# Performance work log

Measured on AMD Instinct MI355X. Metric: run time of the kernel, lower is better.

Reference implementation:

```python
import jax, jax.numpy as jnp
import numpy as np

D_MODEL = 1024
N_HEADS = 16
D_HEAD = D_MODEL // N_HEADS


def setup_inputs() -> dict:
    key = jax.random.key(0)
    ks = jax.random.split(key, 7)
    x = jax.random.normal(ks[0], (1, 4096, D_MODEL), dtype=jnp.float32)
    # torch Linear default init ~ U(-1/sqrt(fan_in), 1/sqrt(fan_in)); small randn is fine for a reference
    Wqkv = jax.random.normal(ks[1], (3 * D_MODEL, D_MODEL), dtype=jnp.float32) * (1.0 / np.sqrt(D_MODEL))
    bqkv = jax.random.normal(ks[2], (3 * D_MODEL,), dtype=jnp.float32) * 0.01
    Wo = jax.random.normal(ks[3], (D_MODEL, D_MODEL), dtype=jnp.float32) * (1.0 / np.sqrt(D_MODEL))
    bo = jax.random.normal(ks[4], (D_MODEL,), dtype=jnp.float32) * 0.01
    wq = jnp.ones((D_HEAD,), dtype=jnp.float32)
    wk = jnp.ones((D_HEAD,), dtype=jnp.float32)
    return {"x": x, "Wqkv": Wqkv, "bqkv": bqkv, "Wo": Wo, "bo": bo, "wq": wq, "wk": wk}


def _rmsnorm(x, w):
    # matches RMSNormRef: mean of squares over last dim, eps added to mean before sqrt
    xf = x.astype(jnp.float32)
    rms = jnp.mean(xf * xf, axis=-1, keepdims=True)
    return (xf / jnp.sqrt(rms + 1e-6) * w.astype(jnp.float32)).astype(x.dtype)


def reference(x, Wqkv, bqkv, Wo, bo, wq, wk):
    b, s, d = x.shape
    qkv = x @ Wqkv.T + bqkv                       # [b, s, 3d]
    q, k, v = jnp.split(qkv, 3, axis=-1)
    q = q.reshape(b, s, N_HEADS, D_HEAD)
    k = k.reshape(b, s, N_HEADS, D_HEAD)
    v = v.reshape(b, s, N_HEADS, D_HEAD)
    q = _rmsnorm(q, wq)
    k = _rmsnorm(k, wk)
    # NOTE: original applies NO 1/sqrt(d_head) scaling and NO causal mask
    qf = q.astype(jnp.float32)
    kf = k.astype(jnp.float32)
    vf = v.astype(jnp.float32)
    attn = jnp.einsum('bqhd,bkhd->bhqk', qf, kf)  # [b, h, s, s] fp32 scores
    attn = jax.nn.softmax(attn, axis=-1)
    z = jnp.einsum('bhqk,bkhd->bqhd', attn, vf).astype(x.dtype)
    z = z.reshape(b, s, d)
    return z @ Wo.T + bo
```

## Files before the change

### kernel.cpp

```cpp
#include <hip/hip_runtime.h>
#include <hip/hip_bf16.h>

typedef __bf16 bf16;
typedef bf16 bf16x8 __attribute__((ext_vector_type(8)));
typedef bf16 bf16x4 __attribute__((ext_vector_type(4)));
typedef float f32x4 __attribute__((ext_vector_type(4)));
typedef float f32x16 __attribute__((ext_vector_type(16)));
typedef unsigned int u32;
typedef u32 u32x4 __attribute__((ext_vector_type(4)));

static constexpr int SEQ    = 4096;
static constexpr int DMODEL = 1024;
static constexpr int NHEADS = 16;
static constexpr int DHEAD  = 64;
static constexpr int QKV3   = 3 * DMODEL;
static constexpr float SMAX = 64.0f;
static constexpr float LOG2E = 1.44269504088896341f;

__device__ inline void gld16(const bf16* g, bf16* l) {
    __builtin_amdgcn_global_load_lds(
        (const __attribute__((address_space(1))) void*)g,
        (__attribute__((address_space(3))) void*)l, 16, 0, 0);
}

__device__ inline bf16x8 load8(const float* src) {
    float4 a = *(const float4*)(src);
    float4 b = *(const float4*)(src + 4);
    bf16x8 r;
    r[0] = (bf16)a.x; r[1] = (bf16)a.y; r[2] = (bf16)a.z; r[3] = (bf16)a.w;
    r[4] = (bf16)b.x; r[5] = (bf16)b.y; r[6] = (bf16)b.z; r[7] = (bf16)b.w;
    return r;
}

__device__ inline f32x16 zero16() {
    f32x16 r;
#pragma unroll
    for (int i = 0; i < 16; ++i) r[i] = 0.f;
    return r;
}

static constexpr size_t NX = (size_t)SEQ * DMODEL;
static constexpr size_t NW = (size_t)QKV3 * DMODEL;
static constexpr size_t NO = (size_t)DMODEL * DMODEL;

__global__ __launch_bounds__(256)
void cvt_all(const float* __restrict__ x, const float* __restrict__ Wqkv,
             const float* __restrict__ Wo, bf16* __restrict__ outbase) {
    const size_t e = ((size_t)blockIdx.x * 256 + threadIdx.x) * 8;
    const float* src;
    if (e < NX)            src = x + e;
    else if (e < NX + NW)  src = Wqkv + (e - NX);
    else                   src = Wo + (e - NX - NW);
    *(bf16x8*)(outbase + e) = load8(src);
}

__global__ __launch_bounds__(256)
void gemm_qkv(const bf16* __restrict__ A, const bf16* __restrict__ W,
              const float* __restrict__ bias, const float* __restrict__ wq,
              const float* __restrict__ wk, bf16* __restrict__ qkv,
              bf16* __restrict__ Vt) {
    __shared__ __align__(16) bf16 As[128 * 32];
    __shared__ __align__(16) bf16 Ws[128 * 32];
    const int tid  = threadIdx.x;
    const int wave = tid >> 6;
    const int ll   = tid & 15;
    const int quad = (tid & 63) >> 4;
    const int wm   = (wave >> 1) * 64;
    const int wn   = (wave & 1) * 64;
    const int m0 = blockIdx.y * 128;
    const int n0 = blockIdx.x * 128;

    f32x4 acc[4][4];
#pragma unroll
    for (int i = 0; i < 4; ++i)
#pragma unroll
        for (int j = 0; j < 4; ++j) acc[i][j] = (f32x4){0.f, 0.f, 0.f, 0.f};

    for (int k0 = 0; k0 < DMODEL; k0 += 32) {
        __syncthreads();
#pragma unroll
        for (int i = 0; i < 2; ++i) {
            const int idx = i * 256 + tid;
            const int row = idx >> 2;
            const int c   = (idx & 3) ^ ((row >> 1) & 3);
            gld16(&A[(size_t)(m0 + row) * DMODEL + k0 + c * 8], As + idx * 8);
            gld16(&W[(size_t)(n0 + row) * DMODEL + k0 + c * 8], Ws + idx * 8);
        }
        __syncthreads();
        bf16x8 af[4], bfr[4];
#pragma unroll
        for (int mi = 0; mi < 4; ++mi) {
            const int row = wm + mi * 16 + ll;
            af[mi] = *(const bf16x8*)(As + (row * 4 + (quad ^ ((ll >> 1) & 3))) * 8);
        }
#pragma unroll
        for (int ni = 0; ni < 4; ++ni) {
            const int row = wn + ni * 16 + ll;
            bfr[ni] = *(const bf16x8*)(Ws + (row * 4 + (quad ^ ((ll >> 1) & 3))) * 8);
        }
#pragma unroll
        for (int mi = 0; mi < 4; ++mi)
#pragma unroll
            for (int ni = 0; ni < 4; ++ni)
                acc[mi][ni] = __builtin_amdgcn_mfma_f32_16x16x32_bf16(
                    af[mi], bfr[ni], acc[mi][ni], 0, 0, 0);
    }

    float bvn[4];
#pragma unroll
    for (int ni = 0; ni < 4; ++ni) bvn[ni] = bias[n0 + wn + ni * 16 + ll];

    const int sect = (n0 + wn) >> 10;
    if (sect < 2) {
        const float* wv = sect ? wk : wq;
        float wvl[4];
#pragma unroll
        for (int ni = 0; ni < 4; ++ni) wvl[ni] = wv[ni * 16 + ll];
#pragma unroll
        for (int mi = 0; mi < 4; ++mi)
#pragma unroll
            for (int r = 0; r < 4; ++r) {
                float xf[4];
                float ss = 0.f;
#pragma unroll
                for (int ni = 0; ni < 4; ++ni) {
                    xf[ni] = (float)(bf16)(acc[mi][ni][r] + bvn[ni]);
                    ss += xf[ni] * xf[ni];
                }
#pragma unroll
                for (int off = 1; off < 16; off <<= 1) ss += __shfl_xor(ss, off);
                const float scale = rsqrtf(ss * (1.0f / 64.0f) + 1e-6f);
                const int row = m0 + wm + mi * 16 + quad * 4 + r;
#pragma unroll
                for (int ni = 0; ni < 4; ++ni)
                    qkv[(size_t)row * QKV3 + n0 + wn + ni * 16 + ll] =
                        (bf16)(xf[ni] * scale * wvl[ni]);
            }
    } else {
        const int h = (n0 + wn - 2 * DMODEL) >> 6;
#pragma unroll
        for (int mi = 0; mi < 4; ++mi) {
            const int kv = m0 + wm + mi * 16 + quad * 4;
#pragma unroll
            for (int ni = 0; ni < 4; ++ni) {
                bf16x4 vv;
#pragma unroll
                for (int r = 0; r < 4; ++r) vv[r] = (bf16)(acc[mi][ni][r] + bvn[ni]);
                *(bf16x4*)(Vt + (size_t)(h * DHEAD + ni * 16 + ll) * SEQ + kv) = vv;
            }
        }
    }
}

__global__ __launch_bounds__(256)
void gemm_out(const bf16* __restrict__ A, const bf16* __restrict__ W,
              const float* __restrict__ bias, float* __restrict__ C) {
    __shared__ __align__(16) bf16 As[128 * 32];
    __shared__ __align__(16) bf16 Ws[64 * 32];
    const int tid  = threadIdx.x;
    const int wave = tid >> 6;
    const int ll   = tid & 15;
    const int quad = (tid & 63) >> 4;
    const int m0 = blockIdx.y * 128;
    const int n0 = blockIdx.x * 64;

    f32x4 acc[2][4];
#pragma unroll
    for (int i = 0; i < 2; ++i)
#pragma unroll
        for (int j = 0; j < 4; ++j) acc[i][j] = (f32x4){0.f, 0.f, 0.f, 0.f};

    for (int k0 = 0; k0 < DMODEL; k0 += 32) {
        __syncthreads();
#pragma unroll
        for (int i = 0; i < 2; ++i) {
            const int idx = i * 256 + tid;
            const int row = idx >> 2;
            const int c   = (idx & 3) ^ ((row >> 1) & 3);
            gld16(&A[(size_t)(m0 + row) * DMODEL + k0 + c * 8], As + idx * 8);
        }
        {
            const int j   = tid;
            const int row = j >> 2;
            const int c   = (j & 3) ^ ((row >> 1) & 3);
            gld16(&W[(size_t)(n0 + row) * DMODEL + k0 + c * 8], Ws + j * 8);
        }
        __syncthreads();
        bf16x8 af[2], bfr[4];
#pragma unroll
        for (int mi = 0; mi < 2; ++mi) {
            const int row = wave * 32 + mi * 16 + ll;
            af[mi] = *(const bf16x8*)(As + (row * 4 + (quad ^ ((ll >> 1) & 3))) * 8);
        }
#pragma unroll
        for (int ni = 0; ni < 4; ++ni) {
            const int row = ni * 16 + ll;
            bfr[ni] = *(const bf16x8*)(Ws + (row * 4 + (quad ^ ((ll >> 1) & 3))) * 8);
        }
#pragma unroll
        for (int mi = 0; mi < 2; ++mi)
#pragma unroll
            for (int ni = 0; ni < 4; ++ni)
                acc[mi][ni] = __builtin_amdgcn_mfma_f32_16x16x32_bf16(
                    af[mi], bfr[ni], acc[mi][ni], 0, 0, 0);
    }
#pragma unroll
    for (int ni = 0; ni < 4; ++ni) {
        const int col = n0 + ni * 16 + ll;
        const float bv = bias[col];
#pragma unroll
        for (int mi = 0; mi < 2; ++mi)
#pragma unroll
            for (int r = 0; r < 4; ++r) {
                const int row = m0 + wave * 32 + mi * 16 + quad * 4 + r;
                C[(size_t)row * DMODEL + col] = acc[mi][ni][r] + bv;
            }
    }
}

template<int NSPLIT>
__global__ __launch_bounds__(256, 2)
void attn_fwd(const bf16* __restrict__ qkv, const bf16* __restrict__ Vt,
              bf16* __restrict__ z, float* __restrict__ opf,
              float* __restrict__ lsum) {
    constexpr bool PARTIAL = (NSPLIT > 1);
    __shared__ __align__(16) bf16 KV[2][2][64 * 64];
    float (*Os)[32][36] = (float(*)[32][36])(&KV[0][0][0]);
    bf16* Qs = &KV[0][0][0];

    const int tid  = threadIdx.x;
    const int wave = tid >> 6;
    const int lane = tid & 63;
    const int l31  = lane & 31;
    const int hh   = lane >> 5;
    const int l7   = lane & 7;
    const int head = blockIdx.x;
    const int q0   = blockIdx.y * 256;
    const int half = PARTIAL ? blockIdx.z : 0;
    const int kvlen = SEQ / NSPLIT;
    const int kvbeg = half * kvlen;
    const int nt    = kvlen / 64;

    const bf16* kbase  = qkv + DMODEL + head * DHEAD;
    const bf16* vtbase = Vt + (size_t)head * DHEAD * SEQ;

    auto stage_kv = [&](int buf, int kv0) {
#pragma unroll
        for (int i = 0; i < 2; ++i) {
            const int idx = i * 256 + tid;
            const int row = idx >> 3;
            const int c   = (idx & 7) ^ (row & 7);
            gld16(kbase + (size_t)(kv0 + row) * QKV3 + c * 8, &KV[buf][0][0] + idx * 8);
            gld16(vtbase + (size_t)row * SEQ + kv0 + c * 8, &KV[buf][1][0] + idx * 8);
        }
    };

#pragma unroll
    for (int i = 0; i < 8; ++i) {
        const int idx = i * 256 + tid;
        const int row = idx >> 3;
        const int c   = (idx & 7) ^ (row & 7);
        gld16(qkv + (size_t)(q0 + row) * QKV3 + head * DHEAD + c * 8, Qs + idx * 8);
    }
    __syncthreads();
    bf16x8 qf[4][2];
#pragma unroll
    for (int kd = 0; kd < 4; ++kd)
#pragma unroll
        for (int qs = 0; qs < 2; ++qs) {
            const int row = wave * 64 + qs * 32 + l31;
            qf[kd][qs] = *(const bf16x8*)(Qs + (row * 8 + ((kd * 2 + hh) ^ l7)) * 8);
        }
    __syncthreads();
    stage_kv(0, kvbeg);
    __syncthreads();

    f32x16 o[2][2];
    o[0][0] = zero16(); o[0][1] = zero16();
    o[1][0] = zero16(); o[1][1] = zero16();
    float lpa[2][4] = {{0.f, 0.f, 0.f, 0.f}, {0.f, 0.f, 0.f, 0.f}};

    int cur = 0;
    for (int t = 0; t < nt; ++t) {
        if (t + 1 < nt) stage_kv(cur ^ 1, kvbeg + (t + 1) * 64);
        const bf16* Ks  = &KV[cur][0][0];
        const bf16* VTs = &KV[cur][1][0];

#pragma unroll
        for (int kvt = 0; kvt < 2; ++kvt) {
            f32x16 st0 = zero16(), st1 = zero16();
            __builtin_amdgcn_s_setprio(1);
#pragma unroll
            for (int kd = 0; kd < 4; ++kd) {
                bf16x8 kf = *(const bf16x8*)(
                    Ks + ((kvt * 32 + l31) * 8 + ((kd * 2 + hh) ^ l7)) * 8);
                st0 = __builtin_amdgcn_mfma_f32_32x32x16_bf16(kf, qf[kd][0], st0, 0, 0, 0);
                st1 = __builtin_amdgcn_mfma_f32_32x32x16_bf16(kf, qf[kd][1], st1, 0, 0, 0);
            }
            __builtin_amdgcn_s_setprio(0);

            float pf0[16], pf1[16];
#pragma unroll
            for (int r = 0; r < 16; ++r)
                pf0[r] = __builtin_amdgcn_exp2f(
                    __builtin_fmaf(st0[r], LOG2E, -SMAX * LOG2E));
#pragma unroll
            for (int r = 0; r < 16; ++r)
                pf1[r] = __builtin_amdgcn_exp2f(
                    __builtin_fmaf(st1[r], LOG2E, -SMAX * LOG2E));
#pragma unroll
            for (int r = 0; r < 16; ++r) lpa[0][r & 3] += pf0[r];
#pragma unroll
            for (int r = 0; r < 16; ++r) lpa[1][r & 3] += pf1[r];

#pragma unroll
            for (int cc = 0; cc < 2; ++cc) {
                u32 a1, b1, a2, b2, a3, b3, a4, b4;
                asm("v_cvt_pk_bf16_f32 %0, %1, %2" : "=v"(a1) : "v"(pf0[8 * cc + 0]), "v"(pf0[8 * cc + 1]));
                asm("v_cvt_pk_bf16_f32 %0, %1, %2" : "=v"(b1) : "v"(pf0[8 * cc + 4]), "v"(pf0[8 * cc + 5]));
                asm("v_cvt_pk_bf16_f32 %0, %1, %2" : "=v"(a2) : "v"(pf0[8 * cc + 2]), "v"(pf0[8 * cc + 3]));
                asm("v_cvt_pk_bf16_f32 %0, %1, %2" : "=v"(b2) : "v"(pf0[8 * cc + 6]), "v"(pf0[8 * cc + 7]));
                asm("v_permlane32_swap_b32 %0, %1" : "+v"(a1), "+v"(b1));
                asm("v_permlane32_swap_b32 %0, %1" : "+v"(a2), "+v"(b2));
                asm("v_cvt_pk_bf16_f32 %0, %1, %2" : "=v"(a3) : "v"(pf1[8 * cc + 0]), "v"(pf1[8 * cc + 1]));
                asm("v_cvt_pk_bf16_f32 %0, %1, %2" : "=v"(b3) : "v"(pf1[8 * cc + 4]), "v"(pf1[8 * cc + 5]));
                asm("v_cvt_pk_bf16_f32 %0, %1, %2" : "=v"(a4) : "v"(pf1[8 * cc + 2]), "v"(pf1[8 * cc + 3]));
                asm("v_cvt_pk_bf16_f32 %0, %1, %2" : "=v"(b4) : "v"(pf1[8 * cc + 6]), "v"(pf1[8 * cc + 7]));
                asm("v_permlane32_swap_b32 %0, %1" : "+v"(a3), "+v"(b3));
                asm("v_permlane32_swap_b32 %0, %1" : "+v"(a4), "+v"(b4));
                u32x4 w0, w1;
                w0[0] = a1; w0[1] = a2; w0[2] = b1; w0[3] = b2;
                w1[0] = a3; w1[1] = a4; w1[2] = b3; w1[3] = b4;
                const bf16x8 bp0 = *(const bf16x8*)&w0;
                const bf16x8 bp1 = *(const bf16x8*)&w1;
                const int c = kvt * 2 + cc;
                __builtin_amdgcn_s_setprio(1);
#pragma unroll
                for (int dt = 0; dt < 2; ++dt) {
                    bf16x8 vf = *(const bf16x8*)(
                        VTs + ((dt * 32 + l31) * 8 + ((c * 2 + hh) ^ l7)) * 8);
                    o[dt][0] = __builtin_amdgcn_mfma_f32_32x32x16_bf16(vf, bp0, o[dt][0], 0, 0, 0);
                    o[dt][1] = __builtin_amdgcn_mfma_f32_32x32x16_bf16(vf, bp1, o[dt][1], 0, 0, 0);
                }
                __builtin_amdgcn_s_setprio(0);
            }
        }
        __syncthreads();
        cur ^= 1;
    }

#pragma unroll
    for (int qs = 0; qs < 2; ++qs) {
        float lp = (lpa[qs][0] + lpa[qs][1]) + (lpa[qs][2] + lpa[qs][3]);
        lp += __shfl_xor(lp, 32);
        const int qrow = q0 + wave * 64 + qs * 32 + l31;
        if (PARTIAL) {
            if (lane < 32) lsum[((size_t)half * SEQ + qrow) * NHEADS + head] = lp;
        }
        const float inv = PARTIAL ? 1.0f : 1.0f / lp;

#pragma unroll
        for (int dt = 0; dt < 2; ++dt) {
#pragma unroll
            for (int r = 0; r < 16; ++r) {
                const int dl = (r & 3) + 8 * (r >> 2) + 4 * hh;
                Os[wave][l31][dl] = o[dt][qs][r] * inv;
            }
#pragma unroll
            for (int it = 0; it < 4; ++it) {
                const int qr  = it * 8 + (lane >> 3);
                const int dl2 = (lane & 7) * 4;
                const f32x4 v = *(const f32x4*)(&Os[wave][qr][dl2]);
                const int row = q0 + wave * 64 + qs * 32 + qr;
                const int col = head * DHEAD + dt * 32 + dl2;
                if (PARTIAL) {
                    *(f32x4*)(opf + ((size_t)half * SEQ + row) * DMODEL + col) = v;
                } else {
                    bf16x4 ov;
                    ov[0] = (bf16)v[0]; ov[1] = (bf16)v[1];
                    ov[2] = (bf16)v[2]; ov[3] = (bf16)v[3];
                    *(bf16x4*)(z + (size_t)row * DMODEL + col) = ov;
                }
            }
        }
    }
}

template<int NS>
__global__ __launch_bounds__(256)
void combine_halves(const float* __restrict__ opf, const float* __restrict__ lsum,
                    bf16* __restrict__ z) {
    const int row = blockIdx.x;
    const int c   = threadIdx.x * 4;
    const int head = c >> 6;
    float l = 0.f;
#pragma unroll
    for (int s = 0; s < NS; ++s)
        l += lsum[((size_t)s * SEQ + row) * NHEADS + head];
    float4 acc = {0.f, 0.f, 0.f, 0.f};
#pragma unroll
    for (int s = 0; s < NS; ++s) {
        const float4 ov = *(const float4*)(opf + ((size_t)s * SEQ + row) * DMODEL + c);
        acc.x += ov.x; acc.y += ov.y; acc.z += ov.z; acc.w += ov.w;
    }
    bf16x4 out;
    out[0] = (bf16)(acc.x / l);
    out[1] = (bf16)(acc.y / l);
    out[2] = (bf16)(acc.z / l);
    out[3] = (bf16)(acc.w / l);
    *(bf16x4*)(z + (size_t)row * DMODEL + c) = out;
}

extern "C" void kernel_launch(void* const* d_in, const int* in_sizes, int n_in,
                              void* d_out, int out_size, void* d_ws, size_t ws_size,
                              hipStream_t stream) {
    const float* x    = (const float*)d_in[0];
    const float* Wqkv = (const float*)d_in[1];
    const float* bqkv = (const float*)d_in[2];
    const float* Wo   = (const float*)d_in[3];
    const float* bo   = (const float*)d_in[4];
    const float* wq   = (const float*)d_in[5];
    const float* wk   = (const float*)d_in[6];
    float* out = (float*)d_out;

    bf16* qkv  = (bf16*)d_ws;
    bf16* z    = qkv + (size_t)SEQ * QKV3;
    bf16* Vt   = z + (size_t)SEQ * DMODEL;
    bf16* xb   = Vt + (size_t)NHEADS * DHEAD * SEQ;
    bf16* Wqb  = xb + NX;
    bf16* Wob  = Wqb + NW;
    bf16* endb = Wob + NO;
    float* opf  = (float*)endb;
    float* lsum4 = opf + (size_t)4 * SEQ * DMODEL;
    float* lsum2 = opf + (size_t)2 * SEQ * DMODEL;
    const size_t need4 = (size_t)((char*)(lsum4 + (size_t)4 * SEQ * NHEADS) - (char*)d_ws);
    const size_t need2 = (size_t)((char*)(lsum2 + (size_t)2 * SEQ * NHEADS) - (char*)d_ws);

    cvt_all<<<dim3((NX + NW + NO) / 2048), 256, 0, stream>>>(x, Wqkv, Wo, xb);

    gemm_qkv<<<dim3(QKV3 / 128, SEQ / 128), 256, 0, stream>>>(
        xb, Wqb, bqkv, wq, wk, qkv, Vt);

    if (ws_size >= need4) {
        attn_fwd<4><<<dim3(NHEADS, SEQ / 256, 4), 256, 0, stream>>>(
            qkv, Vt, z, opf, lsum4);
        combine_halves<4><<<dim3(SEQ), 256, 0, stream>>>(opf, lsum4, z);
    } else if (ws_size >= need2) {
        attn_fwd<2><<<dim3(NHEADS, SEQ / 256, 2), 256, 0, stream>>>(
            qkv, Vt, z, opf, lsum2);
        combine_halves<2><<<dim3(SEQ), 256, 0, stream>>>(opf, lsum2, z);
    } else {
        attn_fwd<1><<<dim3(NHEADS, SEQ / 256, 1), 256, 0, stream>>>(
            qkv, Vt, z, nullptr, nullptr);
    }

    gemm_out<<<dim3(DMODEL / 64, SEQ / 128), 256, 0, stream>>>(z, Wob, bo, out);
}
```

Measured before the change: 242.0 us.

## Double GEMM K-tile to 64 with 8-way swizzle and drop 4-way attention split

Both projection GEMMs now stage 64-wide K tiles in shared memory with a new XOR swizzle over 8 chunks. This halves the number of barrier pairs per K sweep and lets each wave issue two MFMA batches per sync, at the cost of twice the LDS per block. Separately, the 4-way KV split of attention is removed, so it falls back to the 2-way split. That reduces the partial-output traffic and combine work but cuts attention grid parallelism in half.

```diff
diff --git a/kernel.cpp b/kernel.cpp
--- a/kernel.cpp
+++ b/kernel.cpp
@@ -59,8 +59,8 @@
               const float* __restrict__ bias, const float* __restrict__ wq,
               const float* __restrict__ wk, bf16* __restrict__ qkv,
               bf16* __restrict__ Vt) {
-    __shared__ __align__(16) bf16 As[128 * 32];
-    __shared__ __align__(16) bf16 Ws[128 * 32];
+    __shared__ __align__(16) bf16 As[128 * 64];
+    __shared__ __align__(16) bf16 Ws[128 * 64];
     const int tid  = threadIdx.x;
     const int wave = tid >> 6;
     const int ll   = tid & 15;
@@ -76,34 +76,39 @@
 #pragma unroll
         for (int j = 0; j < 4; ++j) acc[i][j] = (f32x4){0.f, 0.f, 0.f, 0.f};
 
-    for (int k0 = 0; k0 < DMODEL; k0 += 32) {
+    for (int k0 = 0; k0 < DMODEL; k0 += 64) {
         __syncthreads();
 #pragma unroll
-        for (int i = 0; i < 2; ++i) {
+        for (int i = 0; i < 4; ++i) {
             const int idx = i * 256 + tid;
-            const int row = idx >> 2;
-            const int c   = (idx & 3) ^ ((row >> 1) & 3);
+            const int row = idx >> 3;
+            const int c   = (idx & 7) ^ (row & 7);
             gld16(&A[(size_t)(m0 + row) * DMODEL + k0 + c * 8], As + idx * 8);
             gld16(&W[(size_t)(n0 + row) * DMODEL + k0 + c * 8], Ws + idx * 8);
         }
         __syncthreads();
-        bf16x8 af[4], bfr[4];
-#pragma unroll
-        for (int mi = 0; mi < 4; ++mi) {
-            const int row = wm + mi * 16 + ll;
-            af[mi] = *(const bf16x8*)(As + (row * 4 + (quad ^ ((ll >> 1) & 3))) * 8);
-        }
-#pragma unroll
-        for (int ni = 0; ni < 4; ++ni) {
-            const int row = wn + ni * 16 + ll;
-            bfr[ni] = *(const bf16x8*)(Ws + (row * 4 + (quad ^ ((ll >> 1) & 3))) * 8);
-        }
-#pragma unroll
-        for (int mi = 0; mi < 4; ++mi)
-#pragma unroll
-            for (int ni = 0; ni < 4; ++ni)
-                acc[mi][ni] = __builtin_amdgcn_mfma_f32_16x16x32_bf16(
-                    af[mi], bfr[ni], acc[mi][ni], 0, 0, 0);
+#pragma unroll
+        for (int kk = 0; kk < 2; ++kk) {
+            bf16x8 af[4], bfr[4];
+#pragma unroll
+            for (int mi = 0; mi < 4; ++mi) {
+                const int row = wm + mi * 16 + ll;
+                const int p   = (kk * 4 + quad) ^ (ll & 7);
+                af[mi] = *(const bf16x8*)(As + (row * 8 + p) * 8);
+            }
+#pragma unroll
+            for (int ni = 0; ni < 4; ++ni) {
+                const int row = wn + ni * 16 + ll;
+                const int p   = (kk * 4 + quad) ^ (ll & 7);
+                bfr[ni] = *(const bf16x8*)(Ws + (row * 8 + p) * 8);
+            }
+#pragma unroll
+            for (int mi = 0; mi < 4; ++mi)
+#pragma unroll
+                for (int ni = 0; ni < 4; ++ni)
+                    acc[mi][ni] = __builtin_amdgcn_mfma_f32_16x16x32_bf16(
+                        af[mi], bfr[ni], acc[mi][ni], 0, 0, 0);
+        }
     }
 
     float bvn[4];
@@ -155,8 +160,8 @@
 __global__ __launch_bounds__(256)
 void gemm_out(const bf16* __restrict__ A, const bf16* __restrict__ W,
               const float* __restrict__ bias, float* __restrict__ C) {
-    __shared__ __align__(16) bf16 As[128 * 32];
-    __shared__ __align__(16) bf16 Ws[64 * 32];
+    __shared__ __align__(16) bf16 As[128 * 64];
+    __shared__ __align__(16) bf16 Ws[64 * 64];
     const int tid  = threadIdx.x;
     const int wave = tid >> 6;
     const int ll   = tid & 15;
@@ -170,39 +175,45 @@
 #pragma unroll
         for (int j = 0; j < 4; ++j) acc[i][j] = (f32x4){0.f, 0.f, 0.f, 0.f};
 
-    for (int k0 = 0; k0 < DMODEL; k0 += 32) {
+    for (int k0 = 0; k0 < DMODEL; k0 += 64) {
         __syncthreads();
+#pragma unroll
+        for (int i = 0; i < 4; ++i) {
+            const int idx = i * 256 + tid;
+            const int row = idx >> 3;
+            const int c   = (idx & 7) ^ (row & 7);
+            gld16(&A[(size_t)(m0 + row) * DMODEL + k0 + c * 8], As + idx * 8);
+        }
 #pragma unroll
         for (int i = 0; i < 2; ++i) {
             const int idx = i * 256 + tid;
-            const int row = idx >> 2;
-            const int c   = (idx & 3) ^ ((row >> 1) & 3);
-            gld16(&A[(size_t)(m0 + row) * DMODEL + k0 + c * 8], As + idx * 8);
-        }
-        {
-            const int j   = tid;
-            const int row = j >> 2;
-            const int c   = (j & 3) ^ ((row >> 1) & 3);
-            gld16(&W[(size_t)(n0 + row) * DMODEL + k0 + c * 8], Ws + j * 8);
+            const int row = idx >> 3;
+            const int c   = (idx & 7) ^ (row & 7);
+            gld16(&W[(size_t)(n0 + row) * DMODEL + k0 + c * 8], Ws + idx * 8);
         }
         __syncthreads();
-        bf16x8 af[2], bfr[4];
-#pragma unroll
-        for (int mi = 0; mi < 2; ++mi) {
-            const int row = wave * 32 + mi * 16 + ll;
-            af[mi] = *(const bf16x8*)(As + (row * 4 + (quad ^ ((ll >> 1) & 3))) * 8);
-        }
-#pragma unroll
-        for (int ni = 0; ni < 4; ++ni) {
-            const int row = ni * 16 + ll;
-            bfr[ni] = *(const bf16x8*)(Ws + (row * 4 + (quad ^ ((ll >> 1) & 3))) * 8);
-        }
-#pragma unroll
-        for (int mi = 0; mi < 2; ++mi)
-#pragma unroll
-            for (int ni = 0; ni < 4; ++ni)
-                acc[mi][ni] = __builtin_amdgcn_mfma_f32_16x16x32_bf16(
-                    af[mi], bfr[ni], acc[mi][ni], 0, 0, 0);
+#pragma unroll
+        for (int kk = 0; kk < 2; ++kk) {
+            bf16x8 af[2], bfr[4];
+#pragma unroll
+            for (int mi = 0; mi < 2; ++mi) {
+                const int row = wave * 32 + mi * 16 + ll;
+                const int p   = (kk * 4 + quad) ^ (ll & 7);
+                af[mi] = *(const bf16x8*)(As + (row * 8 + p) * 8);
+            }
+#pragma unroll
+            for (int ni = 0; ni < 4; ++ni) {
+                const int row = ni * 16 + ll;
+                const int p   = (kk * 4 + quad) ^ (ll & 7);
+                bfr[ni] = *(const bf16x8*)(Ws + (row * 8 + p) * 8);
+            }
+#pragma unroll
+            for (int mi = 0; mi < 2; ++mi)
+#pragma unroll
+                for (int ni = 0; ni < 4; ++ni)
+                    acc[mi][ni] = __builtin_amdgcn_mfma_f32_16x16x32_bf16(
+                        af[mi], bfr[ni], acc[mi][ni], 0, 0, 0);
+        }
     }
 #pragma unroll
     for (int ni = 0; ni < 4; ++ni) {
@@ -431,9 +442,7 @@
     bf16* Wob  = Wqb + NW;
     bf16* endb = Wob + NO;
     float* opf  = (float*)endb;
-    float* lsum4 = opf + (size_t)4 * SEQ * DMODEL;
     float* lsum2 = opf + (size_t)2 * SEQ * DMODEL;
-    const size_t need4 = (size_t)((char*)(lsum4 + (size_t)4 * SEQ * NHEADS) - (char*)d_ws);
     const size_t need2 = (size_t)((char*)(lsum2 + (size_t)2 * SEQ * NHEADS) - (char*)d_ws);
 
     cvt_all<<<dim3((NX + NW + NO) / 2048), 256, 0, stream>>>(x, Wqkv, Wo, xb);
@@ -441,11 +450,7 @@
     gemm_qkv<<<dim3(QKV3 / 128, SEQ / 128), 256, 0, stream>>>(
         xb, Wqb, bqkv, wq, wk, qkv, Vt);
 
-    if (ws_size >= need4) {
-        attn_fwd<4><<<dim3(NHEADS, SEQ / 256, 4), 256, 0, stream>>>(
-            qkv, Vt, z, opf, lsum4);
-        combine_halves<4><<<dim3(SEQ), 256, 0, stream>>>(opf, lsum4, z);
-    } else if (ws_size >= need2) {
+    if (ws_size >= need2) {
         attn_fwd<2><<<dim3(NHEADS, SEQ / 256, 2), 256, 0, stream>>>(
             qkv, Vt, z, opf, lsum2);
         combine_halves<2><<<dim3(SEQ), 256, 0, stream>>>(opf, lsum2, z);
```

Result: faster. 228.2 us (-5.7%).
